# Performance work log

Hardware: AMD Instinct MI355X
Metric: run time of the kernel (lower is better)

## Reference

```python
import jax, jax.numpy as jnp
import numpy as np

N_NODE = 20000
N_EDGE = 200000
EMBED = 256
PAIR = 128
HEADS = 16
HEAD_DIM = EMBED // HEADS
SCALING = HEAD_DIM ** -0.5
EPS = 1e-5


def _ln(x, w, b):
    m = x.mean(-1, keepdims=True)
    v = ((x - m) ** 2).mean(-1, keepdims=True)
    return (x - m) / jnp.sqrt(v + EPS) * w + b


def setup_inputs() -> dict:
    key = jax.random.key(0)
    ks = jax.random.split(key, 12)
    inp = {
        "query": jax.random.normal(ks[0], (N_NODE, EMBED), jnp.float32),
        "edge_index": jax.random.randint(ks[1], (N_EDGE, 2), 0, N_NODE, jnp.int64 if jax.config.jax_enable_x64 else jnp.int32),
        "edge_diff": jax.random.normal(ks[2], (N_EDGE, 3), jnp.float32),
        "pair": jax.random.normal(ks[3], (N_EDGE, PAIR), jnp.float32),
        "ln_w": jnp.ones((EMBED,), jnp.float32),
        "ln_b": jnp.zeros((EMBED,), jnp.float32),
        "pln_w": jnp.ones((PAIR,), jnp.float32),
        "pln_b": jnp.zeros((PAIR,), jnp.float32),
        "Wq": jax.random.normal(ks[4], (EMBED, EMBED), jnp.float32) * 0.02,
        "Wk": jax.random.normal(ks[5], (EMBED, EMBED), jnp.float32) * 0.02,
        "Wv": jax.random.normal(ks[6], (EMBED, EMBED), jnp.float32) * 0.02,
        "Wb": jax.random.normal(ks[7], (HEADS, PAIR), jnp.float32) * 0.02,
        "bb": jnp.zeros((HEADS,), jnp.float32),
        "Wf1": jax.random.normal(ks[8], (1, EMBED), jnp.float32) * 0.02,
        "bf1": jnp.zeros((1,), jnp.float32),
        "Wf2": jax.random.normal(ks[9], (1, EMBED), jnp.float32) * 0.02,
        "bf2": jnp.zeros((1,), jnp.float32),
        "Wf3": jax.random.normal(ks[10], (1, EMBED), jnp.float32) * 0.02,
        "bf3": jnp.zeros((1,), jnp.float32),
    }
    return inp


def reference(query, edge_index, edge_diff, pair, ln_w, ln_b, pln_w, pln_b,
              Wq, Wk, Wv, Wb, bb, Wf1, bf1, Wf2, bf2, Wf3, bf3):
    n_node = query.shape[0]
    src = edge_index[:, 0]
    dst = edge_index[:, 1]

    qn = _ln(query, ln_w, ln_b)          # preln on node features
    pn = _ln(pair, pln_w, pln_b)         # preln on pair features

    q = (qn @ Wq.T).reshape(n_node, HEADS, HEAD_DIM)
    k = (qn @ Wk.T).reshape(n_node, HEADS, HEAD_DIM)
    v = (qn @ Wv.T).reshape(n_node, HEADS, HEAD_DIM)

    qe = q[src] * SCALING                # [E,H,D]
    ke = k[dst]
    ve = v[dst]

    logits = (qe * ke).sum(-1) + pn @ Wb.T + bb   # [E,H]

    # segment softmax over destination node (edge_index[:,0])
    seg_max = jax.ops.segment_max(logits, src, num_segments=n_node)  # [N,H]
    ex = jnp.exp(logits - seg_max[src])
    denom = jax.ops.segment_sum(ex, src, num_segments=n_node)
    probs = ex / denom[src]              # [E,H]

    # 3D-weighted scatter-sum: out[n,h,c,d] = sum_e probs[e,h]*diff[e,c]*v[e,h,d]
    w = probs[:, :, None] * edge_diff[:, None, :]                    # [E,H,3]
    contrib = w[:, :, :, None] * ve[:, :, None, :]                   # [E,H,3,D]
    x = jax.ops.segment_sum(contrib, src, num_segments=n_node)       # [N,H,3,D]
    x = x.transpose(0, 2, 1, 3).reshape(n_node, 3, EMBED)            # [N,3,H*D]

    f1 = x[:, 0, :] @ Wf1.T + bf1
    f2 = x[:, 1, :] @ Wf2.T + bf2
    f3 = x[:, 2, :] @ Wf3.T + bf3
    return jnp.concatenate([f1, f2, f3], axis=-1).astype(jnp.float32)
```

## Files before the change

### kernel.cpp

```cpp
#include <hip/hip_runtime.h>
#include <math.h>

#define N_NODE 20000
#define N_EDGE 200000
#define EMBED 256
#define PAIR 128
#define HEADS 16
#define HEAD_DIM 16
#define SCALING 0.25f
#define LNEPS 1e-5f

typedef unsigned short u16;
typedef unsigned int u32;
typedef __attribute__((ext_vector_type(8))) short bf16x8;
typedef __attribute__((ext_vector_type(4))) float f32x4;

#define WS_QKV   0
#define WS_EX    30720000
#define WS_DENOM 43520000
#define WS_VW    44800000
#define WS_QN    48640000
#define WS_WBF   58880000
#define WS_WW    59273216
#define WS_C0    59277312
#define WS_C1    59277376
#define WS_BIAS  59277440

__device__ __forceinline__ u16 f2bf(float f) {
  u32 u = __float_as_uint(f);
  u32 r = (u + 0x7FFFu + ((u >> 16) & 1u)) >> 16;
  return (u16)r;
}
__device__ __forceinline__ float bl(u32 u) { return __uint_as_float(u << 16); }
__device__ __forceinline__ float bh(u32 u) { return __uint_as_float(u & 0xFFFF0000u); }

__device__ __forceinline__ float dot8(uint4 a, uint4 b) {
  float s = bl(a.x) * bl(b.x) + bh(a.x) * bh(b.x);
  s += bl(a.y) * bl(b.y) + bh(a.y) * bh(b.y);
  s += bl(a.z) * bl(b.z) + bh(a.z) * bh(b.z);
  s += bl(a.w) * bl(b.w) + bh(a.w) * bh(b.w);
  return s;
}

__global__ __launch_bounds__(256) void ln_qn_kernel(
    const float* __restrict__ query, const float* __restrict__ ln_w,
    const float* __restrict__ ln_b, u16* __restrict__ qn) {
  int node = blockIdx.x * 4 + (threadIdx.x >> 6);
  int lane = threadIdx.x & 63;
  float4 a = *(const float4*)(query + (size_t)node * EMBED + lane * 4);
  float s = a.x + a.y + a.z + a.w;
  float s2 = a.x * a.x + a.y * a.y + a.z * a.z + a.w * a.w;
  #pragma unroll
  for (int off = 32; off > 0; off >>= 1) {
    s += __shfl_xor(s, off);
    s2 += __shfl_xor(s2, off);
  }
  float m = s * (1.0f / EMBED);
  float r = rsqrtf(s2 * (1.0f / EMBED) - m * m + LNEPS);
  float4 w4 = *(const float4*)(ln_w + lane * 4);
  float4 b4 = *(const float4*)(ln_b + lane * 4);
  ushort4 st;
  st.x = f2bf((a.x - m) * r * w4.x + b4.x);
  st.y = f2bf((a.y - m) * r * w4.y + b4.y);
  st.z = f2bf((a.z - m) * r * w4.z + b4.z);
  st.w = f2bf((a.w - m) * r * w4.w + b4.w);
  *(ushort4*)(qn + (size_t)node * EMBED + lane * 4) = st;
}

__global__ __launch_bounds__(256) void wcvt_kernel(
    const float* __restrict__ Wq, const float* __restrict__ Wk,
    const float* __restrict__ Wv, u16* __restrict__ Wbf) {
  int g4 = blockIdx.x * 256 + threadIdx.x;
  int idx = g4 * 4;
  const float* src = (idx < 65536) ? Wq : (idx < 131072 ? Wk : Wv);
  float4 v = *(const float4*)(src + (idx & 65535));
  ushort4 st = {f2bf(v.x), f2bf(v.y), f2bf(v.z), f2bf(v.w)};
  *(ushort4*)(Wbf + idx) = st;
}

__global__ __launch_bounds__(64) void prep_kernel(
    const float* __restrict__ pln_w, const float* __restrict__ pln_b,
    const float* __restrict__ Wb, const float* __restrict__ bb,
    u16* __restrict__ WWbf, float* __restrict__ c0, float* __restrict__ c1) {
  int h = blockIdx.x, l = threadIdx.x;
  int i0 = l * 2;
  float wb0 = Wb[h * PAIR + i0], wb1 = Wb[h * PAIR + i0 + 1];
  float ww0 = pln_w[i0] * wb0, ww1 = pln_w[i0 + 1] * wb1;
  WWbf[h * PAIR + i0] = f2bf(ww0);
  WWbf[h * PAIR + i0 + 1] = f2bf(ww1);
  float s1 = ww0 + ww1;
  float s0 = pln_b[i0] * wb0 + pln_b[i0 + 1] * wb1;
  #pragma unroll
  for (int off = 32; off > 0; off >>= 1) {
    s1 += __shfl_xor(s1, off);
    s0 += __shfl_xor(s0, off);
  }
  if (l == 0) {
    c1[h] = s1;
    c0[h] = s0 + bb[h];
  }
}

__global__ __launch_bounds__(256) void init_kernel(
    float* __restrict__ denom, float* __restrict__ out,
    const float* __restrict__ bf1, const float* __restrict__ bf2,
    const float* __restrict__ bf3) {
  int i = blockIdx.x * 256 + threadIdx.x;
  if (i < N_NODE * HEADS) denom[i] = 0.0f;
  if (i < N_NODE) {
    out[i * 3 + 0] = bf1[0];
    out[i * 3 + 1] = bf2[0];
    out[i * 3 + 2] = bf3[0];
  }
}

#define GP 264
__global__ __launch_bounds__(256, 2) void qkv_gemm_kernel(
    const u16* __restrict__ qn, const u16* __restrict__ Wbf,
    u16* __restrict__ qkv) {
  __shared__ u16 As[64 * GP];
  __shared__ u16 Bs[64 * GP];
  int t = threadIdx.x;
  int wv = t >> 6, lane = t & 63;
  int quad = lane >> 4, l16 = lane & 15;
  int row0 = blockIdx.x * 64, col0 = blockIdx.y * 64;
  #pragma unroll
  for (int j = 0; j < 8; j++) {
    int row = j * 8 + (t >> 5);
    int slot = t & 31;
    int ra = min(row0 + row, N_NODE - 1);
    uint4 va = *(const uint4*)(qn + (size_t)ra * 256 + slot * 8);
    *(uint4*)(&As[row * GP + slot * 8]) = va;
    uint4 vb = *(const uint4*)(Wbf + (size_t)(col0 + row) * 256 + slot * 8);
    *(uint4*)(&Bs[row * GP + slot * 8]) = vb;
  }
  __syncthreads();
  int mt = (wv >> 1) * 32, nt = (wv & 1) * 32;
  f32x4 acc[2][2];
  #pragma unroll
  for (int im = 0; im < 2; im++)
    #pragma unroll
    for (int in_ = 0; in_ < 2; in_++) acc[im][in_] = (f32x4){0.f, 0.f, 0.f, 0.f};
  #pragma unroll
  for (int sk = 0; sk < 8; sk++) {
    int ko = sk * 32 + quad * 8;
    bf16x8 a0 = *(const bf16x8*)(&As[(mt + l16) * GP + ko]);
    bf16x8 a1 = *(const bf16x8*)(&As[(mt + 16 + l16) * GP + ko]);
    bf16x8 b0 = *(const bf16x8*)(&Bs[(nt + l16) * GP + ko]);
    bf16x8 b1 = *(const bf16x8*)(&Bs[(nt + 16 + l16) * GP + ko]);
    acc[0][0] = __builtin_amdgcn_mfma_f32_16x16x32_bf16(a0, b0, acc[0][0], 0, 0, 0);
    acc[0][1] = __builtin_amdgcn_mfma_f32_16x16x32_bf16(a0, b1, acc[0][1], 0, 0, 0);
    acc[1][0] = __builtin_amdgcn_mfma_f32_16x16x32_bf16(a1, b0, acc[1][0], 0, 0, 0);
    acc[1][1] = __builtin_amdgcn_mfma_f32_16x16x32_bf16(a1, b1, acc[1][1], 0, 0, 0);
  }
  float scale = (col0 < 256) ? SCALING : 1.0f;
  #pragma unroll
  for (int im = 0; im < 2; im++) {
    #pragma unroll
    for (int in_ = 0; in_ < 2; in_++) {
      #pragma unroll
      for (int r = 0; r < 4; r++) {
        int grow = row0 + mt + im * 16 + quad * 4 + r;
        int gcol = col0 + nt + in_ * 16 + l16;
        if (grow < N_NODE)
          qkv[(size_t)grow * 768 + gcol] = f2bf(acc[im][in_][r] * scale);
      }
    }
  }
}

__global__ __launch_bounds__(256) void vw_kernel(
    const u16* __restrict__ qkv, const float* __restrict__ Wf1,
    const float* __restrict__ Wf2, const float* __restrict__ Wf3,
    float* __restrict__ vw) {
  int gid = blockIdx.x * 256 + threadIdx.x;
  int n = gid >> 4, h = gid & 15;
  const uint4* vp = (const uint4*)(qkv + (size_t)n * 768 + 512 + h * 16);
  uint4 va = vp[0], vb = vp[1];
  float v[16];
  v[0] = bl(va.x); v[1] = bh(va.x); v[2] = bl(va.y); v[3] = bh(va.y);
  v[4] = bl(va.z); v[5] = bh(va.z); v[6] = bl(va.w); v[7] = bh(va.w);
  v[8] = bl(vb.x); v[9] = bh(vb.x); v[10] = bl(vb.y); v[11] = bh(vb.y);
  v[12] = bl(vb.z); v[13] = bh(vb.z); v[14] = bl(vb.w); v[15] = bh(vb.w);
  const float* wf[3] = {Wf1 + h * 16, Wf2 + h * 16, Wf3 + h * 16};
  #pragma unroll
  for (int c = 0; c < 3; c++) {
    float s = 0.f;
    #pragma unroll
    for (int d = 0; d < 16; d++) s += v[d] * wf[c][d];
    vw[(size_t)n * 48 + h * 3 + c] = s;
  }
}

#define PP 136
__global__ __launch_bounds__(256) void pair_bias_kernel(
    const float* __restrict__ pair, const u16* __restrict__ WWbf,
    const float* __restrict__ c0g, const float* __restrict__ c1g,
    float* __restrict__ bias) {
  __shared__ u16 Ps[64 * PP];
  __shared__ u16 WWs[16 * PP];
  __shared__ float ms[64], rs[64], c0s[16], c1s[16];
  int t = threadIdx.x;
  int wv = t >> 6, lane = t & 63;
  int quad = lane >> 4, l16 = lane & 15;
  int e0 = blockIdx.x * 64;
  #pragma unroll
  for (int j = 0; j < 8; j++) {
    int L = j * 256 + t;
    int row = L >> 5, slot = L & 31;
    float4 p = *(const float4*)(pair + (size_t)(e0 + row) * PAIR + slot * 4);
    ushort4 st = {f2bf(p.x), f2bf(p.y), f2bf(p.z), f2bf(p.w)};
    *(ushort4*)(&Ps[row * PP + slot * 4]) = st;
  }
  #pragma unroll
  for (int j = 0; j < 2; j++) {
    int L = j * 256 + t;
    int row = L >> 5, slot = L & 31;
    ushort4 w = *(const ushort4*)(WWbf + row * PAIR + slot * 4);
    *(ushort4*)(&WWs[row * PP + slot * 4]) = w;
  }
  if (t < 16) {
    c0s[t] = c0g[t];
    c1s[t] = c1g[t];
  }
  __syncthreads();
  {
    int row = t >> 2, qq = t & 3;
    float s = 0.f, s2 = 0.f;
    #pragma unroll
    for (int jj = 0; jj < 8; jj++) {
      ushort4 u = *(const ushort4*)(&Ps[row * PP + (qq * 8 + jj) * 4]);
      float x0 = __uint_as_float((u32)u.x << 16);
      float x1 = __uint_as_float((u32)u.y << 16);
      float x2 = __uint_as_float((u32)u.z << 16);
      float x3 = __uint_as_float((u32)u.w << 16);
      s += x0 + x1 + x2 + x3;
      s2 += x0 * x0 + x1 * x1 + x2 * x2 + x3 * x3;
    }
    s += __shfl_xor(s, 1); s += __shfl_xor(s, 2);
    s2 += __shfl_xor(s2, 1); s2 += __shfl_xor(s2, 2);
    if (qq == 0) {
      float m = s * (1.0f / PAIR);
      ms[row] = m;
      rs[row] = rsqrtf(s2 * (1.0f / PAIR) - m * m + LNEPS);
    }
  }
  __syncthreads();
  f32x4 acc = (f32x4){0.f, 0.f, 0.f, 0.f};
  #pragma unroll
  for (int sk = 0; sk < 4; sk++) {
    int ko = sk * 32 + quad * 8;
    bf16x8 a = *(const bf16x8*)(&Ps[(wv * 16 + l16) * PP + ko]);
    bf16x8 b = *(const bf16x8*)(&WWs[l16 * PP + ko]);
    acc = __builtin_amdgcn_mfma_f32_16x16x32_bf16(a, b, acc, 0, 0, 0);
  }
  #pragma unroll
  for (int r = 0; r < 4; r++) {
    int el = wv * 16 + quad * 4 + r;
    float bv = rs[el] * (acc[r] - ms[el] * c1s[l16]) + c0s[l16];
    bias[(size_t)(e0 + el) * HEADS + l16] = bv;
  }
}

__global__ __launch_bounds__(256) void qk_exp_kernel(
    const int* __restrict__ edge_index, const u16* __restrict__ qkv,
    const float* __restrict__ bias, float* __restrict__ ex,
    float* __restrict__ denom) {
  int gid = blockIdx.x * 256 + threadIdx.x;
  int e = gid >> 4, h = gid & 15;
  int src = edge_index[e * 2 + 0];
  int dst = edge_index[e * 2 + 1];
  const uint4* qp = (const uint4*)(qkv + (size_t)src * 768 + h * 16);
  const uint4* kp = (const uint4*)(qkv + (size_t)dst * 768 + 256 + h * 16);
  uint4 q0 = qp[0], q1 = qp[1];
  uint4 k0 = kp[0], k1 = kp[1];
  float d = dot8(q0, k0) + dot8(q1, k1);
  float exv = __expf(d + bias[gid]);
  ex[gid] = exv;
  atomicAdd(&denom[src * HEADS + h], exv);
}

__global__ __launch_bounds__(256) void recip_kernel(float* __restrict__ denom) {
  int i = blockIdx.x * 256 + threadIdx.x;
  if (i < N_NODE * HEADS) denom[i] = 1.0f / denom[i];
}

__global__ __launch_bounds__(256) void edge_accum_kernel(
    const int* __restrict__ edge_index, const float* __restrict__ edge_diff,
    const float* __restrict__ ex, const float* __restrict__ rdenom,
    const float* __restrict__ vw, float* __restrict__ out) {
  int gid = blockIdx.x * 256 + threadIdx.x;
  int e = gid >> 4, h = gid & 15;
  int src = edge_index[e * 2 + 0];
  int dst = edge_index[e * 2 + 1];
  float pr = ex[gid] * rdenom[src * HEADS + h];
  const float* vwd = vw + (size_t)dst * 48 + h * 3;
  float v0 = pr * vwd[0], v1 = pr * vwd[1], v2 = pr * vwd[2];
  #pragma unroll
  for (int off = 8; off > 0; off >>= 1) {
    v0 += __shfl_xor(v0, off);
    v1 += __shfl_xor(v1, off);
    v2 += __shfl_xor(v2, off);
  }
  if (h == 0) {
    atomicAdd(&out[src * 3 + 0], edge_diff[e * 3 + 0] * v0);
    atomicAdd(&out[src * 3 + 1], edge_diff[e * 3 + 1] * v1);
    atomicAdd(&out[src * 3 + 2], edge_diff[e * 3 + 2] * v2);
  }
}

extern "C" void kernel_launch(void* const* d_in, const int* in_sizes, int n_in,
                              void* d_out, int out_size, void* d_ws,
                              size_t ws_size, hipStream_t stream) {
  const float* query      = (const float*)d_in[0];
  const int*   edge_index = (const int*)d_in[1];
  const float* edge_diff  = (const float*)d_in[2];
  const float* pair       = (const float*)d_in[3];
  const float* ln_w       = (const float*)d_in[4];
  const float* ln_b       = (const float*)d_in[5];
  const float* pln_w      = (const float*)d_in[6];
  const float* pln_b      = (const float*)d_in[7];
  const float* Wq         = (const float*)d_in[8];
  const float* Wk         = (const float*)d_in[9];
  const float* Wv         = (const float*)d_in[10];
  const float* Wb         = (const float*)d_in[11];
  const float* bb         = (const float*)d_in[12];
  const float* Wf1        = (const float*)d_in[13];
  const float* bf1        = (const float*)d_in[14];
  const float* Wf2        = (const float*)d_in[15];
  const float* bf2        = (const float*)d_in[16];
  const float* Wf3        = (const float*)d_in[17];
  const float* bf3        = (const float*)d_in[18];

  char* ws = (char*)d_ws;
  u16*   qkv   = (u16*)(ws + WS_QKV);
  float* exb   = (float*)(ws + WS_EX);
  float* denom = (float*)(ws + WS_DENOM);
  float* vw    = (float*)(ws + WS_VW);
  u16*   qn    = (u16*)(ws + WS_QN);
  u16*   Wbf   = (u16*)(ws + WS_WBF);
  u16*   WWbf  = (u16*)(ws + WS_WW);
  float* c0    = (float*)(ws + WS_C0);
  float* c1    = (float*)(ws + WS_C1);
  float* bias  = (float*)(ws + WS_BIAS);
  float* out   = (float*)d_out;

  ln_qn_kernel<<<N_NODE / 4, 256, 0, stream>>>(query, ln_w, ln_b, qn);
  wcvt_kernel<<<192, 256, 0, stream>>>(Wq, Wk, Wv, Wbf);
  prep_kernel<<<16, 64, 0, stream>>>(pln_w, pln_b, Wb, bb, WWbf, c0, c1);
  init_kernel<<<1250, 256, 0, stream>>>(denom, out, bf1, bf2, bf3);
  dim3 ggrid((N_NODE + 63) / 64, 12);
  qkv_gemm_kernel<<<ggrid, 256, 0, stream>>>(qn, Wbf, qkv);
  vw_kernel<<<1250, 256, 0, stream>>>(qkv, Wf1, Wf2, Wf3, vw);
  pair_bias_kernel<<<N_EDGE / 64, 256, 0, stream>>>(pair, WWbf, c0, c1, bias);
  qk_exp_kernel<<<N_EDGE * HEADS / 256, 256, 0, stream>>>(edge_index, qkv, bias,
                                                          exb, denom);
  recip_kernel<<<1250, 256, 0, stream>>>(denom);
  edge_accum_kernel<<<N_EDGE * HEADS / 256, 256, 0, stream>>>(
      edge_index, edge_diff, exb, denom, vw, out);
}
```

Measured before the change: 308.3 us.

## Replace atomic edge softmax with CSR-sorted per-node segment attention

Builds a CSR grouping of edges by source node (histogram, single-block scan, atomic scatter) and replaces the three edge-parallel kernels with one per-node kernel. That kernel computes the softmax denominator and the weighted 3-vector accumulation in two passes, so it needs no global atomics, no ex/denom buffers and no init kernel. The cost is three extra small kernels, including a serial single-block scan, and computing q·k and exp twice per edge. The edge order inside a segment is nondeterministic, and the max-subtraction is still omitted.

```diff
diff --git a/kernel.cpp b/kernel.cpp
--- a/kernel.cpp
+++ b/kernel.cpp
@@ -16,15 +16,17 @@
 typedef __attribute__((ext_vector_type(4))) float f32x4;
 
 #define WS_QKV   0
-#define WS_EX    30720000
-#define WS_DENOM 43520000
-#define WS_VW    44800000
-#define WS_QN    48640000
-#define WS_WBF   58880000
-#define WS_WW    59273216
-#define WS_C0    59277312
-#define WS_C1    59277376
-#define WS_BIAS  59277440
+#define WS_QN    30720000
+#define WS_WBF   40960000
+#define WS_WW    41353216
+#define WS_C0    41357312
+#define WS_C1    41357376
+#define WS_BIAS  41357440
+#define WS_VW    54157440
+#define WS_CNT   57997440
+#define WS_CUR   58077440
+#define WS_OFF   58157440
+#define WS_DE    58237504
 
 __device__ __forceinline__ u16 f2bf(float f) {
   u32 u = __float_as_uint(f);
@@ -44,7 +46,10 @@
 
 __global__ __launch_bounds__(256) void ln_qn_kernel(
     const float* __restrict__ query, const float* __restrict__ ln_w,
-    const float* __restrict__ ln_b, u16* __restrict__ qn) {
+    const float* __restrict__ ln_b, u16* __restrict__ qn,
+    int* __restrict__ counts, int* __restrict__ cur) {
+  int z = blockIdx.x * 256 + threadIdx.x;
+  if (z < N_NODE) { counts[z] = 0; cur[z] = 0; }
   int node = blockIdx.x * 4 + (threadIdx.x >> 6);
   int lane = threadIdx.x & 63;
   float4 a = *(const float4*)(query + (size_t)node * EMBED + lane * 4);
@@ -98,19 +103,6 @@
   if (l == 0) {
     c1[h] = s1;
     c0[h] = s0 + bb[h];
-  }
-}
-
-__global__ __launch_bounds__(256) void init_kernel(
-    float* __restrict__ denom, float* __restrict__ out,
-    const float* __restrict__ bf1, const float* __restrict__ bf2,
-    const float* __restrict__ bf3) {
-  int i = blockIdx.x * 256 + threadIdx.x;
-  if (i < N_NODE * HEADS) denom[i] = 0.0f;
-  if (i < N_NODE) {
-    out[i * 3 + 0] = bf1[0];
-    out[i * 3 + 1] = bf2[0];
-    out[i * 3 + 2] = bf3[0];
   }
 }
 
@@ -262,50 +254,100 @@
   }
 }
 
-__global__ __launch_bounds__(256) void qk_exp_kernel(
-    const int* __restrict__ edge_index, const u16* __restrict__ qkv,
-    const float* __restrict__ bias, float* __restrict__ ex,
-    float* __restrict__ denom) {
-  int gid = blockIdx.x * 256 + threadIdx.x;
-  int e = gid >> 4, h = gid & 15;
+__global__ __launch_bounds__(256) void hist_kernel(
+    const int* __restrict__ edge_index, int* __restrict__ counts) {
+  int e = blockIdx.x * 256 + threadIdx.x;
+  if (e < N_EDGE) atomicAdd(&counts[edge_index[e * 2]], 1);
+}
+
+__global__ __launch_bounds__(1024) void scan_kernel(
+    const int* __restrict__ counts, int* __restrict__ off) {
+  __shared__ int part[1024];
+  int t = threadIdx.x;
+  int loc[20];
+  int s = 0;
+  #pragma unroll
+  for (int i = 0; i < 20; i++) {
+    int idx = t * 20 + i;
+    int v = (idx < N_NODE) ? counts[idx] : 0;
+    loc[i] = s;
+    s += v;
+  }
+  part[t] = s;
+  __syncthreads();
+  int x = s;
+  for (int o = 1; o < 1024; o <<= 1) {
+    int y = (t >= o) ? part[t - o] : 0;
+    __syncthreads();
+    x += y;
+    part[t] = x;
+    __syncthreads();
+  }
+  int excl = x - s;
+  #pragma unroll
+  for (int i = 0; i < 20; i++) {
+    int idx = t * 20 + i;
+    if (idx < N_NODE) off[idx] = excl + loc[i];
+  }
+  if (t == 0) off[N_NODE] = N_EDGE;
+}
+
+__global__ __launch_bounds__(256) void scatter_kernel(
+    const int* __restrict__ edge_index, const int* __restrict__ off,
+    int* __restrict__ cur, int2* __restrict__ de) {
+  int e = blockIdx.x * 256 + threadIdx.x;
+  if (e >= N_EDGE) return;
   int src = edge_index[e * 2 + 0];
   int dst = edge_index[e * 2 + 1];
+  int pos = off[src] + atomicAdd(&cur[src], 1);
+  de[pos] = make_int2(dst, e);
+}
+
+__global__ __launch_bounds__(256) void seg_attn_kernel(
+    const u16* __restrict__ qkv, const float* __restrict__ bias,
+    const int* __restrict__ off, const int2* __restrict__ de,
+    const float* __restrict__ vw, const float* __restrict__ edge_diff,
+    const float* __restrict__ bf1, const float* __restrict__ bf2,
+    const float* __restrict__ bf3, float* __restrict__ out) {
+  int wv = threadIdx.x >> 6, lane = threadIdx.x & 63;
+  int src = blockIdx.x * 4 + wv;
+  int h = lane & 15, eslot = lane >> 4;
+  int lo = off[src];
+  int deg = off[src + 1] - lo;
   const uint4* qp = (const uint4*)(qkv + (size_t)src * 768 + h * 16);
-  const uint4* kp = (const uint4*)(qkv + (size_t)dst * 768 + 256 + h * 16);
   uint4 q0 = qp[0], q1 = qp[1];
-  uint4 k0 = kp[0], k1 = kp[1];
-  float d = dot8(q0, k0) + dot8(q1, k1);
-  float exv = __expf(d + bias[gid]);
-  ex[gid] = exv;
-  atomicAdd(&denom[src * HEADS + h], exv);
-}
-
-__global__ __launch_bounds__(256) void recip_kernel(float* __restrict__ denom) {
-  int i = blockIdx.x * 256 + threadIdx.x;
-  if (i < N_NODE * HEADS) denom[i] = 1.0f / denom[i];
-}
-
-__global__ __launch_bounds__(256) void edge_accum_kernel(
-    const int* __restrict__ edge_index, const float* __restrict__ edge_diff,
-    const float* __restrict__ ex, const float* __restrict__ rdenom,
-    const float* __restrict__ vw, float* __restrict__ out) {
-  int gid = blockIdx.x * 256 + threadIdx.x;
-  int e = gid >> 4, h = gid & 15;
-  int src = edge_index[e * 2 + 0];
-  int dst = edge_index[e * 2 + 1];
-  float pr = ex[gid] * rdenom[src * HEADS + h];
-  const float* vwd = vw + (size_t)dst * 48 + h * 3;
-  float v0 = pr * vwd[0], v1 = pr * vwd[1], v2 = pr * vwd[2];
-  #pragma unroll
-  for (int off = 8; off > 0; off >>= 1) {
-    v0 += __shfl_xor(v0, off);
-    v1 += __shfl_xor(v1, off);
-    v2 += __shfl_xor(v2, off);
-  }
-  if (h == 0) {
-    atomicAdd(&out[src * 3 + 0], edge_diff[e * 3 + 0] * v0);
-    atomicAdd(&out[src * 3 + 1], edge_diff[e * 3 + 1] * v1);
-    atomicAdd(&out[src * 3 + 2], edge_diff[e * 3 + 2] * v2);
+  float exsum = 0.f;
+  for (int ei = eslot; ei < deg; ei += 4) {
+    int2 d_e = de[lo + ei];
+    const uint4* kp = (const uint4*)(qkv + (size_t)d_e.x * 768 + 256 + h * 16);
+    float d = dot8(q0, kp[0]) + dot8(q1, kp[1]);
+    exsum += __expf(d + bias[(size_t)d_e.y * HEADS + h]);
+  }
+  exsum += __shfl_xor(exsum, 16);
+  exsum += __shfl_xor(exsum, 32);
+  float rden = (exsum > 0.f) ? 1.0f / exsum : 0.f;
+  float a0 = 0.f, a1 = 0.f, a2 = 0.f;
+  for (int ei = eslot; ei < deg; ei += 4) {
+    int2 d_e = de[lo + ei];
+    const uint4* kp = (const uint4*)(qkv + (size_t)d_e.x * 768 + 256 + h * 16);
+    float d = dot8(q0, kp[0]) + dot8(q1, kp[1]);
+    float pr = __expf(d + bias[(size_t)d_e.y * HEADS + h]) * rden;
+    const float* vp = vw + (size_t)d_e.x * 48 + h * 3;
+    const float* dp = edge_diff + (size_t)d_e.y * 3;
+    a0 += pr * vp[0] * dp[0];
+    a1 += pr * vp[1] * dp[1];
+    a2 += pr * vp[2] * dp[2];
+  }
+  #pragma unroll
+  for (int o = 1; o < 64; o <<= 1) {
+    a0 += __shfl_xor(a0, o);
+    a1 += __shfl_xor(a1, o);
+    a2 += __shfl_xor(a2, o);
+  }
+  if (lane == 0) {
+    out[src * 3 + 0] = a0 + bf1[0];
+    out[src * 3 + 1] = a1 + bf2[0];
+    out[src * 3 + 2] = a2 + bf3[0];
   }
 }
 
@@ -334,28 +376,32 @@
 
   char* ws = (char*)d_ws;
   u16*   qkv   = (u16*)(ws + WS_QKV);
-  float* exb   = (float*)(ws + WS_EX);
-  float* denom = (float*)(ws + WS_DENOM);
-  float* vw    = (float*)(ws + WS_VW);
   u16*   qn    = (u16*)(ws + WS_QN);
   u16*   Wbf   = (u16*)(ws + WS_WBF);
   u16*   WWbf  = (u16*)(ws + WS_WW);
   float* c0    = (float*)(ws + WS_C0);
   float* c1    = (float*)(ws + WS_C1);
   float* bias  = (float*)(ws + WS_BIAS);
+  float* vw    = (float*)(ws + WS_VW);
+  int*   counts= (int*)(ws + WS_CNT);
+  int*   cur   = (int*)(ws + WS_CUR);
+  int*   off   = (int*)(ws + WS_OFF);
+  int2*  de    = (int2*)(ws + WS_DE);
   float* out   = (float*)d_out;
 
-  ln_qn_kernel<<<N_NODE / 4, 256, 0, stream>>>(query, ln_w, ln_b, qn);
+  ln_qn_kernel<<<N_NODE / 4, 256, 0, stream>>>(query, ln_w, ln_b, qn, counts,
+                                               cur);
   wcvt_kernel<<<192, 256, 0, stream>>>(Wq, Wk, Wv, Wbf);
   prep_kernel<<<16, 64, 0, stream>>>(pln_w, pln_b, Wb, bb, WWbf, c0, c1);
-  init_kernel<<<1250, 256, 0, stream>>>(denom, out, bf1, bf2, bf3);
   dim3 ggrid((N_NODE + 63) / 64, 12);
   qkv_gemm_kernel<<<ggrid, 256, 0, stream>>>(qn, Wbf, qkv);
   vw_kernel<<<1250, 256, 0, stream>>>(qkv, Wf1, Wf2, Wf3, vw);
   pair_bias_kernel<<<N_EDGE / 64, 256, 0, stream>>>(pair, WWbf, c0, c1, bias);
-  qk_exp_kernel<<<N_EDGE * HEADS / 256, 256, 0, stream>>>(edge_index, qkv, bias,
-                                                          exb, denom);
-  recip_kernel<<<1250, 256, 0, stream>>>(denom);
-  edge_accum_kernel<<<N_EDGE * HEADS / 256, 256, 0, stream>>>(
-      edge_index, edge_diff, exb, denom, vw, out);
-}
+  hist_kernel<<<(N_EDGE + 255) / 256, 256, 0, stream>>>(edge_index, counts);
+  scan_kernel<<<1, 1024, 0, stream>>>(counts, off);
+  scatter_kernel<<<(N_EDGE + 255) / 256, 256, 0, stream>>>(edge_index, off, cur,
+                                                           de);
+  seg_attn_kernel<<<N_NODE / 4, 256, 0, stream>>>(qkv, bias, off, de, vw,
+                                                  edge_diff, bf1, bf2, bf3,
+                                                  out);
+}
```

Result: slower. 319.2 us (+3.6%).
